# Performance work log

Hardware: AMD Instinct MI355X
Metric: run time of the kernel (lower is better)

The kernel has to match this reference:

```python
import jax, jax.numpy as jnp
import numpy as np

N = 100_000
E = 1_000_000
D = 64
NORM_FACTOR = 100.0
LN_EPS = 1e-5


def setup_inputs() -> dict:
    key = jax.random.key(0)
    ks = jax.random.split(key, 8)
    h = jax.random.normal(ks[0], (N, D), dtype=jnp.float32)
    distances = jax.random.uniform(ks[1], (E, 1), dtype=jnp.float32)
    edges = jax.random.randint(ks[2], (2, E), 0, N, dtype=jnp.int64)
    node_mask = jnp.ones((N, 1), dtype=jnp.float32)
    edge_mask = jnp.ones((E, 1), dtype=jnp.float32)
    s = 1.0 / np.sqrt(D)
    W_lin = jax.random.normal(ks[3], (D, D), dtype=jnp.float32) * s
    b_lin = jnp.zeros((D,), dtype=jnp.float32)
    att_W1 = jax.random.normal(ks[4], (D, 2 * D + 1), dtype=jnp.float32) * (1.0 / np.sqrt(2 * D + 1))
    att_b1 = jnp.zeros((D,), dtype=jnp.float32)
    att_W2 = jax.random.normal(ks[5], (1, D), dtype=jnp.float32) * s
    att_b2 = jnp.zeros((1,), dtype=jnp.float32)
    ln_g = jnp.ones((D,), dtype=jnp.float32)
    ln_b = jnp.zeros((D,), dtype=jnp.float32)
    return {"h": h, "distances": distances, "edges": edges, "node_mask": node_mask,
            "edge_mask": edge_mask, "W_lin": W_lin, "b_lin": b_lin,
            "att_W1": att_W1, "att_b1": att_b1, "att_W2": att_W2, "att_b2": att_b2,
            "ln_g": ln_g, "ln_b": ln_b}


def reference(h, distances, edges, node_mask, edge_mask, W_lin, b_lin,
              att_W1, att_b1, att_W2, att_b2, ln_g, ln_b):
    # Linear projection: [N, D]
    x = h @ W_lin.T + b_lin
    row, col = edges[0], edges[1]
    x_row = x[row]          # [E, D]
    x_col = x[col]          # [E, D]
    # DenseAtt: MLP(concat(x_row, x_col, dist)) -> sigmoid -> * edge_mask
    cat = jnp.concatenate([x_row, x_col, distances], axis=1)  # [E, 2D+1]
    hdn = jax.nn.silu(cat @ att_W1.T + att_b1)                # [E, D]
    att = jax.nn.sigmoid(hdn @ att_W2.T + att_b2) * edge_mask # [E, 1]
    # Attention-weighted scatter-sum aggregation into row segments
    agg = x_col * att
    out = jax.ops.segment_sum(agg, row, num_segments=x.shape[0]) / NORM_FACTOR
    out = out + x           # residual
    # LayerNorm + activation
    mu = jnp.mean(out, axis=-1, keepdims=True)
    var = jnp.mean(jnp.square(out - mu), axis=-1, keepdims=True)
    y = (out - mu) * jax.lax.rsqrt(var + LN_EPS) * ln_g + ln_b
    return jax.nn.silu(y)
```

## Files before the change

kernel.cpp:

```cpp
#include <hip/hip_runtime.h>
#include <hip/hip_bf16.h>

#define N_NODES 100000
#define N_EDGES 1000000
#define DIM 64
#define NORM_INV 0.01f
#define LN_EPS 1e-5f
#define N_TILES 6250
#define PROJ_BLOCKS 1563
#define N_BUCKETS 782
#define NB_PAD 800
#define SC_EDGES 4096
#define SC_BLOCKS 245
#define OFS_STRIDE 784
#define L2E 1.4426950408889634f
#define LN2 0.6931471805599453f
#define CAP 2560

typedef __attribute__((ext_vector_type(8))) short short8;
typedef __attribute__((ext_vector_type(4))) float f32x4;

__device__ __forceinline__ unsigned short f2bf(float f) {
    union { float f; unsigned u; } x; x.f = f;
    unsigned r = x.u + 0x7FFFu + ((x.u >> 16) & 1u);
    return (unsigned short)(r >> 16);
}
__device__ __forceinline__ float bf2f(unsigned short s) {
    union { unsigned u; float f; } x; x.u = ((unsigned)s) << 16; return x.f;
}

__global__ __launch_bounds__(256) void proj_scatter(
    const float* __restrict__ h, const float* __restrict__ bl,
    const float* __restrict__ W, const float* __restrict__ att_W1,
    const int* __restrict__ edges, const float* __restrict__ dist,
    const float* __restrict__ emask,
    uint2* __restrict__ srec, int* __restrict__ ofsT,
    unsigned short* __restrict__ xv, unsigned short* __restrict__ u_bf) {
    __shared__ __align__(16) char pool[39168];
    __shared__ int wsum[4];

    if (blockIdx.x < SC_BLOCKS) {
        int* lh = (int*)pool;
        int* lofs = (int*)pool + NB_PAD;
        uint2* lsort = (uint2*)(pool + 6400);
        const int blk = blockIdx.x;
        const int tid = threadIdx.x;
        const int lane = tid & 63;
        const int w = tid >> 6;
        for (int i = tid; i < NB_PAD; i += 256) lh[i] = 0;
        __syncthreads();

        const int eb = blk * SC_EDGES;
        const int total = min(SC_EDGES, N_EDGES - eb);

        int rows[16], rank[16];
        uint2 recs[16];
        const int e0 = eb + tid * 16;
#pragma unroll
        for (int g = 0; g < 4; ++g) {
            const int e = e0 + g * 4;
            if (e + 4 <= N_EDGES) {
                const int4 rr = *(const int4*)(edges + e);
                const int4 cc = *(const int4*)(edges + N_EDGES + e);
                const float4 dd = *(const float4*)(dist + e);
                const float4 mm = *(const float4*)(emask + e);
                rows[g*4+0] = rr.x; rows[g*4+1] = rr.y; rows[g*4+2] = rr.z; rows[g*4+3] = rr.w;
                const int c4[4] = {cc.x, cc.y, cc.z, cc.w};
                const float d4[4] = {dd.x, dd.y, dd.z, dd.w};
                const float m4[4] = {mm.x, mm.y, mm.z, mm.w};
#pragma unroll
                for (int i = 0; i < 4; ++i) {
                    const int ii = g * 4 + i;
                    recs[ii].x = (unsigned)c4[i] | ((unsigned)(rows[ii] & 127) << 24);
                    recs[ii].y = (unsigned)f2bf(d4[i]) |
                                 ((unsigned)f2bf(m4[i] * NORM_INV) << 16);
                    rank[ii] = atomicAdd(&lh[rows[ii] >> 7], 1);
                }
            } else {
#pragma unroll
                for (int i = 0; i < 4; ++i) {
                    const int ii = g * 4 + i;
                    const int ee = e + i;
                    if (ee < N_EDGES) {
                        rows[ii] = edges[ee];
                        recs[ii].x = (unsigned)edges[N_EDGES + ee] |
                                     ((unsigned)(rows[ii] & 127) << 24);
                        recs[ii].y = (unsigned)f2bf(dist[ee]) |
                                     ((unsigned)f2bf(emask[ee] * NORM_INV) << 16);
                        rank[ii] = atomicAdd(&lh[rows[ii] >> 7], 1);
                    } else {
                        rows[ii] = -1;
                    }
                }
            }
        }
        __syncthreads();

        const int b0 = tid * 4;
        int c0 = 0, c1 = 0, c2 = 0, c3 = 0;
        if (b0 < NB_PAD) { c0 = lh[b0]; c1 = lh[b0+1]; c2 = lh[b0+2]; c3 = lh[b0+3]; }
        const int S = c0 + c1 + c2 + c3;
        int sc = S;
#pragma unroll
        for (int off = 1; off < 64; off <<= 1) {
            int u = __shfl_up(sc, off);
            if (lane >= off) sc += u;
        }
        if (lane == 63) wsum[w] = sc;
        __syncthreads();
        int wbase = 0;
        if (w > 0) wbase = wsum[0];
        if (w > 1) wbase += wsum[1];
        if (w > 2) wbase += wsum[2];
        const int excl = sc - S + wbase;
        if (b0 < NB_PAD) {
            lofs[b0] = excl;
            lofs[b0+1] = excl + c0;
            lofs[b0+2] = excl + c0 + c1;
            lofs[b0+3] = excl + c0 + c1 + c2;
        }
        __syncthreads();

#pragma unroll
        for (int i = 0; i < 16; ++i) {
            if (rows[i] >= 0) {
                const int bk = rows[i] >> 7;
                lsort[lofs[bk] + rank[i]] = recs[i];
            }
        }
        __syncthreads();

        for (int s = tid; s < total; s += 256)
            srec[(size_t)blk * SC_EDGES + s] = lsort[s];
        for (int b = tid; b < 783; b += 256)
            ofsT[blk * OFS_STRIDE + b] = lofs[b];
        return;
    }

    const int tid = threadIdx.x;
    const int lane = tid & 63;
    const int wv = tid >> 6;
    const int c = lane & 15, q = lane >> 4;

    {
        short8* Lwhi_w = (short8*)pool;
        short8* Lwlo_w = Lwhi_w + 512;
        short8* Lwa_w  = Lwhi_w + 1024;
        short8* Lwb_w  = Lwhi_w + 1536;
        const int nt_b = tid >> 6;
        const int n_b = nt_b * 16 + c;
#pragma unroll
        for (int ks = 0; ks < 2; ++ks) {
            const int k0 = ks * 32 + q * 8;
            short8 hi8, lo8, a8, b8;
#pragma unroll
            for (int jj = 0; jj < 8; ++jj) {
                float w = W[n_b * 64 + k0 + jj];
                unsigned short hh = f2bf(w);
                hi8[jj] = (short)hh;
                lo8[jj] = (short)f2bf(w - bf2f(hh));
                a8[jj] = (short)f2bf(att_W1[n_b * 129 + k0 + jj]);
                b8[jj] = (short)f2bf(att_W1[n_b * 129 + 64 + k0 + jj]);
            }
            const int idx = (nt_b * 2 + ks) * 64 + lane;
            Lwhi_w[idx] = hi8; Lwlo_w[idx] = lo8; Lwa_w[idx] = a8; Lwb_w[idx] = b8;
        }
    }
    __syncthreads();
    const short8* Lwhi = (const short8*)pool;
    const short8* Lwlo = Lwhi + 512;
    const short8* Lwa  = Lwhi + 1024;
    const short8* Lwb  = Lwhi + 1536;

    const int tile = (blockIdx.x - SC_BLOCKS) * 4 + wv;
    const bool valid = (tile < N_TILES);
    const int n0 = valid ? tile * 16 : 0;

    float bias[4];
#pragma unroll
    for (int nt = 0; nt < 4; ++nt) bias[nt] = bl[nt * 16 + c];

    short8 Ahi[2], Alo[2];
#pragma unroll
    for (int ks = 0; ks < 2; ++ks) {
        const float* hp = h + (size_t)(n0 + c) * 64 + ks * 32 + q * 8;
        f32x4 p0 = *(const f32x4*)hp;
        f32x4 p1 = *(const f32x4*)(hp + 4);
        short8 hi8, lo8;
#pragma unroll
        for (int jj = 0; jj < 4; ++jj) {
            unsigned short hh = f2bf(p0[jj]);
            hi8[jj] = (short)hh; lo8[jj] = (short)f2bf(p0[jj] - bf2f(hh));
            unsigned short h2 = f2bf(p1[jj]);
            hi8[4 + jj] = (short)h2; lo8[4 + jj] = (short)f2bf(p1[jj] - bf2f(h2));
        }
        Ahi[ks] = hi8; Alo[ks] = lo8;
    }

    f32x4 xacc[4] = {{0,0,0,0},{0,0,0,0},{0,0,0,0},{0,0,0,0}};
#pragma unroll
    for (int ks = 0; ks < 2; ++ks)
#pragma unroll
        for (int nt = 0; nt < 4; ++nt) {
            const short8 fhi = Lwhi[(nt * 2 + ks) * 64 + lane];
            const short8 flo = Lwlo[(nt * 2 + ks) * 64 + lane];
            xacc[nt] = __builtin_amdgcn_mfma_f32_16x16x32_bf16(Ahi[ks], fhi, xacc[nt], 0, 0, 0);
            xacc[nt] = __builtin_amdgcn_mfma_f32_16x16x32_bf16(Ahi[ks], flo, xacc[nt], 0, 0, 0);
            xacc[nt] = __builtin_amdgcn_mfma_f32_16x16x32_bf16(Alo[ks], fhi, xacc[nt], 0, 0, 0);
        }

    __syncthreads();

    unsigned short* lw = (unsigned short*)pool + wv * (16 * 72);
#pragma unroll
    for (int r = 0; r < 4; ++r) {
        const int node = n0 + q * 4 + r;
        unsigned short xb[4];
#pragma unroll
        for (int nt = 0; nt < 4; ++nt) {
            unsigned short v16 = f2bf(xacc[nt][r] + bias[nt]);
            xb[nt] = v16;
            lw[(q * 4 + r) * 72 + nt * 16 + c] = v16;
        }
        if (valid) {
            uint2 pk;
            pk.x = (unsigned)xb[0] | ((unsigned)xb[1] << 16);
            pk.y = (unsigned)xb[2] | ((unsigned)xb[3] << 16);
            *(uint2*)(xv + (size_t)node * 128 + c * 8) = pk;
        }
    }

    short8 Ax[2];
#pragma unroll
    for (int ks = 0; ks < 2; ++ks)
        Ax[ks] = *(const short8*)&lw[c * 72 + ks * 32 + q * 8];

    f32x4 uacc[4] = {{0,0,0,0},{0,0,0,0},{0,0,0,0},{0,0,0,0}};
    f32x4 vacc[4] = {{0,0,0,0},{0,0,0,0},{0,0,0,0},{0,0,0,0}};
#pragma unroll
    for (int ks = 0; ks < 2; ++ks)
#pragma unroll
        for (int nt = 0; nt < 4; ++nt) {
            const short8 fa = Lwa[(nt * 2 + ks) * 64 + lane];
            const short8 fb = Lwb[(nt * 2 + ks) * 64 + lane];
            uacc[nt] = __builtin_amdgcn_mfma_f32_16x16x32_bf16(Ax[ks], fa, uacc[nt], 0, 0, 0);
            vacc[nt] = __builtin_amdgcn_mfma_f32_16x16x32_bf16(Ax[ks], fb, vacc[nt], 0, 0, 0);
        }
    if (valid) {
#pragma unroll
        for (int r = 0; r < 4; ++r) {
            const int node = n0 + q * 4 + r;
            uint2 pu;
            pu.x = (unsigned)f2bf(uacc[0][r] * L2E) | ((unsigned)f2bf(uacc[1][r] * L2E) << 16);
            pu.y = (unsigned)f2bf(uacc[2][r] * L2E) | ((unsigned)f2bf(uacc[3][r] * L2E) << 16);
            *(uint2*)(u_bf + (size_t)node * 64 + c * 4) = pu;
            uint2 pk;
            pk.x = (unsigned)f2bf(vacc[0][r] * L2E) | ((unsigned)f2bf(vacc[1][r] * L2E) << 16);
            pk.y = (unsigned)f2bf(vacc[2][r] * L2E) | ((unsigned)f2bf(vacc[3][r] * L2E) << 16);
            *(uint2*)(xv + (size_t)node * 128 + c * 8 + 4) = pk;
        }
    }
}

__global__ __launch_bounds__(512, 4) void agg_fused(
    const uint2* __restrict__ srec, const int* __restrict__ ofsT,
    const unsigned short* __restrict__ xv, const unsigned short* __restrict__ u_bf,
    const float* __restrict__ att_W1, const float* __restrict__ att_b1,
    const float* __restrict__ att_W2, const float* __restrict__ att_b2,
    const float* __restrict__ ln_g, const float* __restrict__ ln_b,
    float* __restrict__ out) {
    __shared__ __align__(16) uint2 lrecs[CAP + 16];
    __shared__ float4 ltab[64];
    __shared__ int hist[128];
    __shared__ int rst[129];
    __shared__ int cur[128];
    __shared__ int sst[256];
    __shared__ int dbase[257];
    __shared__ int wsum4[4];
    __shared__ int wtot;

    const int b = blockIdx.x;
    const int tid = threadIdx.x;
    const int lane = tid & 63;
    const int wv = tid >> 6;

    if (tid < 128) hist[tid] = 0;
    if (tid >= 448) {
        const int f = tid - 448;
        ltab[f] = make_float4(att_W2[f] * LN2, att_W1[f * 129 + 128] * L2E,
                              att_b1[f] * L2E, 0.f);
    }

    int stv = 0, len = 0, sc0 = 0;
    if (tid < 256) {
        if (tid < SC_BLOCKS) {
            stv = ofsT[tid * OFS_STRIDE + b];
            len = ofsT[tid * OFS_STRIDE + b + 1] - stv;
        }
        sst[tid] = stv;
        sc0 = len;
#pragma unroll
        for (int off = 1; off < 64; off <<= 1) {
            int u = __shfl_up(sc0, off);
            if (lane >= off) sc0 += u;
        }
        if (lane == 63) wsum4[wv] = sc0;
    }
    __syncthreads();
    if (tid < 256) {
        int wbase = 0;
        if (wv > 0) wbase = wsum4[0];
        if (wv > 1) wbase += wsum4[1];
        if (wv > 2) wbase += wsum4[2];
        dbase[tid] = wbase + sc0 - len;
        if (tid == 255) dbase[256] = wbase + sc0;
    }
    __syncthreads();
    const int cnt = dbase[245];

    uint2 rec0, rec1, rec2, rec3, rec4;
    int lr0 = -1, lr1 = -1, lr2 = -1, lr3 = -1, lr4 = -1;
#define GATHER(I, RC, LR)                                                     \
    {                                                                         \
        const int m = tid + I * 512;                                          \
        if (m < cnt) {                                                        \
            int lo = 0, hi = 245;                                             \
            while (hi - lo > 1) {                                             \
                const int mid = (lo + hi) >> 1;                               \
                if (dbase[mid] <= m) lo = mid; else hi = mid;                 \
            }                                                                 \
            RC = srec[(size_t)lo * SC_EDGES + sst[lo] + (m - dbase[lo])];     \
            LR = (int)(RC.x >> 24);                                           \
            RC.x &= 0x00FFFFFFu;                                              \
            atomicAdd(&hist[LR], 1);                                          \
        }                                                                     \
    }
    GATHER(0, rec0, lr0)
    GATHER(1, rec1, lr1)
    GATHER(2, rec2, lr2)
    GATHER(3, rec3, lr3)
    GATHER(4, rec4, lr4)
#undef GATHER
    __syncthreads();

    int c = 0, p = 0, sc = 0;
    if (tid < 128) {
        c = hist[tid];
        p = (c + 3) & ~3;
        sc = p;
#pragma unroll
        for (int off = 1; off < 64; off <<= 1) {
            int u = __shfl_up(sc, off);
            if (lane >= off) sc += u;
        }
        if (tid == 63) wtot = sc;
    }
    __syncthreads();
    if (tid < 128) {
        if (tid >= 64) sc += wtot;
        const int excl = sc - p;
        rst[tid] = excl;
        cur[tid] = excl;
        uint2 z; z.x = 0; z.y = 0;
        for (int i = c; i < p; ++i) lrecs[excl + i] = z;
        if (tid == 127) {
            rst[128] = excl + p;
            for (int i = 0; i < 16; ++i) lrecs[excl + p + i] = z;
        }
    }
    __syncthreads();

    if (lr0 >= 0) lrecs[atomicAdd(&cur[lr0], 1)] = rec0;
    if (lr1 >= 0) lrecs[atomicAdd(&cur[lr1], 1)] = rec1;
    if (lr2 >= 0) lrecs[atomicAdd(&cur[lr2], 1)] = rec2;
    if (lr3 >= 0) lrecs[atomicAdd(&cur[lr3], 1)] = rec3;
    if (lr4 >= 0) lrecs[atomicAdd(&cur[lr4], 1)] = rec4;
    __syncthreads();

    const int j = lane & 15;
    const int sl = lane >> 4;
    const float4 t0 = ltab[j], t1 = ltab[j + 16], t2 = ltab[j + 32], t3 = ltab[j + 48];
    const float b2L = att_b2[0] * L2E;
    const float gg = ln_g[lane], bb = ln_b[lane];
    const unsigned* xvu = (const unsigned*)xv;

#pragma unroll 1
    for (int k = 0; k < 16; ++k) {
        const int lrw = wv + 8 * k;
        const int r = b * 128 + lrw;
        if (r >= N_NODES) break;

        const uint2 uu = *(const uint2*)(u_bf + (size_t)r * 64 + j * 4);
        const float base0 = __uint_as_float(uu.x << 16) + t0.z;
        const float base1 = __uint_as_float(uu.x & 0xffff0000u) + t1.z;
        const float base2 = __uint_as_float(uu.y << 16) + t2.z;
        const float base3 = __uint_as_float(uu.y & 0xffff0000u) + t3.z;

        const int s0 = rst[lrw];
        const int e1 = rst[lrw + 1];

        float a0 = 0.f, a1 = 0.f, a2 = 0.f, a3 = 0.f;
        if (e1 > s0) {
            uint2 recA = lrecs[s0 + sl];
            uint4 xvA = *(const uint4*)(xvu + (size_t)recA.x * 64 + j * 4);
            for (int e = s0; e < e1; e += 4) {
                const uint2 recB = lrecs[e + 4 + sl];
                const uint4 xvB = *(const uint4*)(xvu + (size_t)recB.x * 64 + j * 4);

                const float dist = __uint_as_float(recA.y << 16);
                const float emN = __uint_as_float(recA.y & 0xffff0000u);
                const float x0 = __uint_as_float(xvA.x << 16);
                const float x1 = __uint_as_float(xvA.x & 0xffff0000u);
                const float x2 = __uint_as_float(xvA.y << 16);
                const float x3 = __uint_as_float(xvA.y & 0xffff0000u);
                const float v0 = __uint_as_float(xvA.z << 16);
                const float v1 = __uint_as_float(xvA.z & 0xffff0000u);
                const float v2 = __uint_as_float(xvA.w << 16);
                const float v3 = __uint_as_float(xvA.w & 0xffff0000u);
                float pv = 0.f, pre, sg;
                pre = fmaf(dist, t0.y, base0) + v0;
                sg = __builtin_amdgcn_rcpf(1.f + __builtin_amdgcn_exp2f(-pre));
                pv = fmaf(pre * sg, t0.x, pv);
                pre = fmaf(dist, t1.y, base1) + v1;
                sg = __builtin_amdgcn_rcpf(1.f + __builtin_amdgcn_exp2f(-pre));
                pv = fmaf(pre * sg, t1.x, pv);
                pre = fmaf(dist, t2.y, base2) + v2;
                sg = __builtin_amdgcn_rcpf(1.f + __builtin_amdgcn_exp2f(-pre));
                pv = fmaf(pre * sg, t2.x, pv);
                pre = fmaf(dist, t3.y, base3) + v3;
                sg = __builtin_amdgcn_rcpf(1.f + __builtin_amdgcn_exp2f(-pre));
                pv = fmaf(pre * sg, t3.x, pv);
                pv += __shfl_xor(pv, 1); pv += __shfl_xor(pv, 2);
                pv += __shfl_xor(pv, 4); pv += __shfl_xor(pv, 8);
                const float sp = fmaf(pv, L2E, b2L);
                const float att =
                    emN * __builtin_amdgcn_rcpf(1.f + __builtin_amdgcn_exp2f(-sp));
                a0 = fmaf(att, x0, a0); a1 = fmaf(att, x1, a1);
                a2 = fmaf(att, x2, a2); a3 = fmaf(att, x3, a3);
                recA = recB; xvA = xvB;
            }
        }
        a0 += __shfl_xor(a0, 16); a0 += __shfl_xor(a0, 32);
        a1 += __shfl_xor(a1, 16); a1 += __shfl_xor(a1, 32);
        a2 += __shfl_xor(a2, 16); a2 += __shfl_xor(a2, 32);
        a3 += __shfl_xor(a3, 16); a3 += __shfl_xor(a3, 32);

        const uint2 xr = *(const uint2*)(xvu + (size_t)r * 64 + j * 4);
        const float o0 = __uint_as_float(xr.x << 16) + a0;
        const float o1 = __uint_as_float(xr.x & 0xffff0000u) + a1;
        const float o2 = __uint_as_float(xr.y << 16) + a2;
        const float o3 = __uint_as_float(xr.y & 0xffff0000u) + a3;

        float ssum = o0 + o1 + o2 + o3;
        ssum += __shfl_xor(ssum, 1); ssum += __shfl_xor(ssum, 2);
        ssum += __shfl_xor(ssum, 4); ssum += __shfl_xor(ssum, 8);
        const float mu = ssum * (1.f / 64.f);
        const float d0 = o0 - mu, d1 = o1 - mu, d2 = o2 - mu, d3 = o3 - mu;
        float vs = d0 * d0 + d1 * d1 + d2 * d2 + d3 * d3;
        vs += __shfl_xor(vs, 1); vs += __shfl_xor(vs, 2);
        vs += __shfl_xor(vs, 4); vs += __shfl_xor(vs, 8);
        const float rstd = rsqrtf(vs * (1.f / 64.f) + LN_EPS);

        const float dk = (sl == 0) ? d0 : (sl == 1) ? d1 : (sl == 2) ? d2 : d3;
        const float y = fmaf(dk * rstd, gg, bb);
        out[(size_t)r * 64 + lane] =
            y * __builtin_amdgcn_rcpf(1.f + __builtin_amdgcn_exp2f(-y * L2E));
    }
}

extern "C" void kernel_launch(void* const* d_in, const int* in_sizes, int n_in,
                              void* d_out, int out_size, void* d_ws, size_t ws_size,
                              hipStream_t stream) {
    const float* h      = (const float*)d_in[0];
    const float* dist   = (const float*)d_in[1];
    const int*   edges  = (const int*)d_in[2];
    const float* emask  = (const float*)d_in[4];
    const float* W_lin  = (const float*)d_in[5];
    const float* b_lin  = (const float*)d_in[6];
    const float* att_W1 = (const float*)d_in[7];
    const float* att_b1 = (const float*)d_in[8];
    const float* att_W2 = (const float*)d_in[9];
    const float* att_b2 = (const float*)d_in[10];
    const float* ln_g   = (const float*)d_in[11];
    const float* ln_b   = (const float*)d_in[12];
    float* out = (float*)d_out;

    char* ws = (char*)d_ws;
    unsigned short* xv   = (unsigned short*)ws;
    unsigned short* u_bf = (unsigned short*)(ws + 25600000);
    uint2* srec          = (uint2*)(ws + 38400000);
    int* ofsT            = (int*)(ws + 46428160);

    proj_scatter<<<SC_BLOCKS + PROJ_BLOCKS, 256, 0, stream>>>(
        h, b_lin, W_lin, att_W1, edges, dist, emask, srec, ofsT, xv, u_bf);
    agg_fused<<<N_BUCKETS, 512, 0, stream>>>(srec, ofsT, xv, u_bf,
                                             att_W1, att_b1, att_W2, att_b2,
                                             ln_g, ln_b, out);
}
```

Before: 197.4 us.

## Halve node bucket size to 64 rows and pack bucket counters as 16-bit pairs

Bucket size drops from 128 nodes to 64, so agg_fused launches twice as many 256-thread blocks with half the shared edge capacity. In the scatter stage, two 16-bit counters and offsets are packed per int so the doubled bucket count fits in the same shared memory. The goal is finer-grained work for better load balance and occupancy on the aggregation kernel. In exchange, each agg block does more per-block setup: it scans all 245 scatter-block offsets and runs a binary search per edge.

```diff
diff --git a/kernel.cpp b/kernel.cpp
--- a/kernel.cpp
+++ b/kernel.cpp
@@ -8,14 +8,14 @@
 #define LN_EPS 1e-5f
 #define N_TILES 6250
 #define PROJ_BLOCKS 1563
-#define N_BUCKETS 782
-#define NB_PAD 800
+#define N_BUCKETS 1563
+#define HB_PK 784
 #define SC_EDGES 4096
 #define SC_BLOCKS 245
-#define OFS_STRIDE 784
+#define OFS_STRIDE 1568
 #define L2E 1.4426950408889634f
 #define LN2 0.6931471805599453f
-#define CAP 2560
+#define CAP 1280
 
 typedef __attribute__((ext_vector_type(8))) short short8;
 typedef __attribute__((ext_vector_type(4))) float f32x4;
@@ -41,13 +41,13 @@
 
     if (blockIdx.x < SC_BLOCKS) {
         int* lh = (int*)pool;
-        int* lofs = (int*)pool + NB_PAD;
-        uint2* lsort = (uint2*)(pool + 6400);
+        int* lofsP = (int*)pool + HB_PK;
+        uint2* lsort = (uint2*)(pool + 6272);
         const int blk = blockIdx.x;
         const int tid = threadIdx.x;
         const int lane = tid & 63;
         const int w = tid >> 6;
-        for (int i = tid; i < NB_PAD; i += 256) lh[i] = 0;
+        for (int i = tid; i < HB_PK; i += 256) lh[i] = 0;
         __syncthreads();
 
         const int eb = blk * SC_EDGES;
@@ -71,10 +71,12 @@
 #pragma unroll
                 for (int i = 0; i < 4; ++i) {
                     const int ii = g * 4 + i;
-                    recs[ii].x = (unsigned)c4[i] | ((unsigned)(rows[ii] & 127) << 24);
+                    recs[ii].x = (unsigned)c4[i] | ((unsigned)(rows[ii] & 63) << 24);
                     recs[ii].y = (unsigned)f2bf(d4[i]) |
                                  ((unsigned)f2bf(m4[i] * NORM_INV) << 16);
-                    rank[ii] = atomicAdd(&lh[rows[ii] >> 7], 1);
+                    const int bk = rows[ii] >> 6;
+                    const int sh = (bk & 1) << 4;
+                    rank[ii] = (atomicAdd(&lh[bk >> 1], 1 << sh) >> sh) & 0xffff;
                 }
             } else {
 #pragma unroll
@@ -84,10 +86,12 @@
                     if (ee < N_EDGES) {
                         rows[ii] = edges[ee];
                         recs[ii].x = (unsigned)edges[N_EDGES + ee] |
-                                     ((unsigned)(rows[ii] & 127) << 24);
+                                     ((unsigned)(rows[ii] & 63) << 24);
                         recs[ii].y = (unsigned)f2bf(dist[ee]) |
                                      ((unsigned)f2bf(emask[ee] * NORM_INV) << 16);
-                        rank[ii] = atomicAdd(&lh[rows[ii] >> 7], 1);
+                        const int bk = rows[ii] >> 6;
+                        const int sh = (bk & 1) << 4;
+                        rank[ii] = (atomicAdd(&lh[bk >> 1], 1 << sh) >> sh) & 0xffff;
                     } else {
                         rows[ii] = -1;
                     }
@@ -96,10 +100,19 @@
         }
         __syncthreads();
 
-        const int b0 = tid * 4;
-        int c0 = 0, c1 = 0, c2 = 0, c3 = 0;
-        if (b0 < NB_PAD) { c0 = lh[b0]; c1 = lh[b0+1]; c2 = lh[b0+2]; c3 = lh[b0+3]; }
-        const int S = c0 + c1 + c2 + c3;
+        const int t4 = tid * 4;
+        int li[4];
+#pragma unroll
+        for (int g = 0; g < 4; ++g) li[g] = (t4 + g < HB_PK) ? lh[t4 + g] : 0;
+        int cs[8];
+#pragma unroll
+        for (int g = 0; g < 4; ++g) {
+            cs[2*g]   = li[g] & 0xffff;
+            cs[2*g+1] = (li[g] >> 16) & 0xffff;
+        }
+        int S = 0;
+#pragma unroll
+        for (int k = 0; k < 8; ++k) S += cs[k];
         int sc = S;
 #pragma unroll
         for (int off = 1; off < 64; off <<= 1) {
@@ -112,28 +125,30 @@
         if (w > 0) wbase = wsum[0];
         if (w > 1) wbase += wsum[1];
         if (w > 2) wbase += wsum[2];
-        const int excl = sc - S + wbase;
-        if (b0 < NB_PAD) {
-            lofs[b0] = excl;
-            lofs[b0+1] = excl + c0;
-            lofs[b0+2] = excl + c0 + c1;
-            lofs[b0+3] = excl + c0 + c1 + c2;
+        int run = sc - S + wbase;
+#pragma unroll
+        for (int g = 0; g < 4; ++g) {
+            const int lo = run; run += cs[2*g];
+            const int hi = run; run += cs[2*g+1];
+            if (t4 + g < HB_PK) lofsP[t4 + g] = (unsigned)lo | ((unsigned)hi << 16);
         }
         __syncthreads();
 
 #pragma unroll
         for (int i = 0; i < 16; ++i) {
             if (rows[i] >= 0) {
-                const int bk = rows[i] >> 7;
-                lsort[lofs[bk] + rank[i]] = recs[i];
+                const int bk = rows[i] >> 6;
+                const int base = (lofsP[bk >> 1] >> ((bk & 1) << 4)) & 0xffff;
+                lsort[base + rank[i]] = recs[i];
             }
         }
         __syncthreads();
 
         for (int s = tid; s < total; s += 256)
             srec[(size_t)blk * SC_EDGES + s] = lsort[s];
-        for (int b = tid; b < 783; b += 256)
-            ofsT[blk * OFS_STRIDE + b] = lofs[b];
+        for (int b = tid; b < 1564; b += 256)
+            ofsT[blk * OFS_STRIDE + b] =
+                (lofsP[b >> 1] >> ((b & 1) << 4)) & 0xffff;
         return;
     }
 
@@ -262,7 +277,7 @@
     }
 }
 
-__global__ __launch_bounds__(512, 4) void agg_fused(
+__global__ __launch_bounds__(256, 8) void agg_fused(
     const uint2* __restrict__ srec, const int* __restrict__ ofsT,
     const unsigned short* __restrict__ xv, const unsigned short* __restrict__ u_bf,
     const float* __restrict__ att_W1, const float* __restrict__ att_b1,
@@ -271,28 +286,27 @@
     float* __restrict__ out) {
     __shared__ __align__(16) uint2 lrecs[CAP + 16];
     __shared__ float4 ltab[64];
-    __shared__ int hist[128];
-    __shared__ int rst[129];
-    __shared__ int cur[128];
+    __shared__ int hist[64];
+    __shared__ int rst[65];
+    __shared__ int cur[64];
     __shared__ int sst[256];
     __shared__ int dbase[257];
     __shared__ int wsum4[4];
-    __shared__ int wtot;
 
     const int b = blockIdx.x;
     const int tid = threadIdx.x;
     const int lane = tid & 63;
     const int wv = tid >> 6;
 
-    if (tid < 128) hist[tid] = 0;
-    if (tid >= 448) {
-        const int f = tid - 448;
+    if (tid < 64) hist[tid] = 0;
+    if (tid >= 192) {
+        const int f = tid - 192;
         ltab[f] = make_float4(att_W2[f] * LN2, att_W1[f * 129 + 128] * L2E,
                               att_b1[f] * L2E, 0.f);
     }
 
     int stv = 0, len = 0, sc0 = 0;
-    if (tid < 256) {
+    {
         if (tid < SC_BLOCKS) {
             stv = ofsT[tid * OFS_STRIDE + b];
             len = ofsT[tid * OFS_STRIDE + b + 1] - stv;
@@ -307,7 +321,7 @@
         if (lane == 63) wsum4[wv] = sc0;
     }
     __syncthreads();
-    if (tid < 256) {
+    {
         int wbase = 0;
         if (wv > 0) wbase = wsum4[0];
         if (wv > 1) wbase += wsum4[1];
@@ -318,11 +332,11 @@
     __syncthreads();
     const int cnt = dbase[245];
 
-    uint2 rec0, rec1, rec2, rec3, rec4;
-    int lr0 = -1, lr1 = -1, lr2 = -1, lr3 = -1, lr4 = -1;
+    uint2 rec0, rec1, rec2, rec3;
+    int lr0 = -1, lr1 = -1, lr2 = -1, lr3 = -1;
 #define GATHER(I, RC, LR)                                                     \
     {                                                                         \
-        const int m = tid + I * 512;                                          \
+        const int m = tid + I * 256;                                          \
         if (m < cnt) {                                                        \
             int lo = 0, hi = 245;                                             \
             while (hi - lo > 1) {                                             \
@@ -339,32 +353,25 @@
     GATHER(1, rec1, lr1)
     GATHER(2, rec2, lr2)
     GATHER(3, rec3, lr3)
-    GATHER(4, rec4, lr4)
 #undef GATHER
     __syncthreads();
 
-    int c = 0, p = 0, sc = 0;
-    if (tid < 128) {
-        c = hist[tid];
-        p = (c + 3) & ~3;
-        sc = p;
+    if (tid < 64) {
+        const int c = hist[tid];
+        const int p = (c + 3) & ~3;
+        int sc = p;
 #pragma unroll
         for (int off = 1; off < 64; off <<= 1) {
             int u = __shfl_up(sc, off);
             if (lane >= off) sc += u;
         }
-        if (tid == 63) wtot = sc;
-    }
-    __syncthreads();
-    if (tid < 128) {
-        if (tid >= 64) sc += wtot;
         const int excl = sc - p;
         rst[tid] = excl;
         cur[tid] = excl;
         uint2 z; z.x = 0; z.y = 0;
         for (int i = c; i < p; ++i) lrecs[excl + i] = z;
-        if (tid == 127) {
-            rst[128] = excl + p;
+        if (tid == 63) {
+            rst[64] = excl + p;
             for (int i = 0; i < 16; ++i) lrecs[excl + p + i] = z;
         }
     }
@@ -374,7 +381,6 @@
     if (lr1 >= 0) lrecs[atomicAdd(&cur[lr1], 1)] = rec1;
     if (lr2 >= 0) lrecs[atomicAdd(&cur[lr2], 1)] = rec2;
     if (lr3 >= 0) lrecs[atomicAdd(&cur[lr3], 1)] = rec3;
-    if (lr4 >= 0) lrecs[atomicAdd(&cur[lr4], 1)] = rec4;
     __syncthreads();
 
     const int j = lane & 15;
@@ -386,8 +392,8 @@
 
 #pragma unroll 1
     for (int k = 0; k < 16; ++k) {
-        const int lrw = wv + 8 * k;
-        const int r = b * 128 + lrw;
+        const int lrw = wv + 4 * k;
+        const int r = b * 64 + lrw;
         if (r >= N_NODES) break;
 
         const uint2 uu = *(const uint2*)(u_bf + (size_t)r * 64 + j * 4);
@@ -493,7 +499,7 @@
 
     proj_scatter<<<SC_BLOCKS + PROJ_BLOCKS, 256, 0, stream>>>(
         h, b_lin, W_lin, att_W1, edges, dist, emask, srec, ofsT, xv, u_bf);
-    agg_fused<<<N_BUCKETS, 512, 0, stream>>>(srec, ofsT, xv, u_bf,
+    agg_fused<<<N_BUCKETS, 256, 0, stream>>>(srec, ofsT, xv, u_bf,
                                              att_W1, att_b1, att_W2, att_b2,
                                              ln_g, ln_b, out);
 }
```

After: 192.3 us. 2.6% less time.
